# Optimization experiments

Measured on AMD Instinct MI355X. Metric: run time of the kernel, lower is better.

The kernel has to match this reference:

```python
import jax, jax.numpy as jnp
import numpy as np

D_MODEL = 1024
N_HEAD = 16
D_HEAD = D_MODEL // N_HEAD


def setup_inputs() -> dict:
    key = jax.random.key(0)
    ks = jax.random.split(key, 5)
    x = jax.random.normal(ks[0], (4, 2048, D_MODEL), dtype=jnp.float32)
    # qkv linear: weight [3*d_model, d_model], bias [3*d_model] (torch convention)
    w_qkv = jax.random.normal(ks[1], (3 * D_MODEL, D_MODEL), dtype=jnp.float32) / np.sqrt(D_MODEL)
    b_qkv = jnp.zeros((3 * D_MODEL,), dtype=jnp.float32)
    w_proj = jax.random.normal(ks[2], (D_MODEL, D_MODEL), dtype=jnp.float32) / np.sqrt(D_MODEL)
    b_proj = jnp.zeros((D_MODEL,), dtype=jnp.float32)
    return {"x": x, "w_qkv": w_qkv, "b_qkv": b_qkv, "w_proj": w_proj, "b_proj": b_proj}


def reference(x, w_qkv, b_qkv, w_proj, b_proj):
    B, T, C = x.shape
    qkv = x @ w_qkv.T + b_qkv  # [B,T,3C]
    q, k, v = jnp.split(qkv, 3, axis=-1)
    # [B, H, T, Dh]
    q = q.reshape(B, T, N_HEAD, D_HEAD).transpose(0, 2, 1, 3)
    k = k.reshape(B, T, N_HEAD, D_HEAD).transpose(0, 2, 1, 3)
    v = v.reshape(B, T, N_HEAD, D_HEAD).transpose(0, 2, 1, 3)
    att = jnp.einsum('bhqd,bhkd->bhqk', q, k) / jnp.sqrt(jnp.float32(D_HEAD))
    causal = jnp.tril(jnp.ones((T, T), dtype=bool))  # [T,T]
    att = jnp.where(causal, att, -jnp.inf)
    att = jax.nn.softmax(att, axis=-1)
    y = jnp.einsum('bhqk,bhkd->bhqd', att, v)  # [B,H,T,Dh]
    y = y.transpose(0, 2, 1, 3).reshape(B, T, C)
    return y @ w_proj.T + b_proj
```

## Files before the change

### kernel.cpp

```cpp
#include <hip/hip_runtime.h>
#include <hip/hip_bf16.h>

#define DEV static __device__ __forceinline__

typedef __attribute__((ext_vector_type(8))) short short8;
typedef __attribute__((ext_vector_type(4))) short short4v;
typedef __attribute__((ext_vector_type(4))) float float4v;
typedef __attribute__((ext_vector_type(4))) int int4v;

DEV unsigned short f2bf(float f) {
  unsigned int u = __builtin_bit_cast(unsigned int, f);
  u = (u + 0x7fffu + ((u >> 16) & 1u)) >> 16;
  return (unsigned short)u;
}

DEV __attribute__((address_space(3))) void* to_lds(void* p) {
  return (__attribute__((address_space(3))) void*)p;
}
DEV const __attribute__((address_space(1))) void* to_glb(const void* p) {
  return (const __attribute__((address_space(1))) void*)p;
}

DEV float4v zero4() { float4v z = {0.f, 0.f, 0.f, 0.f}; return z; }

DEV float ex2(float x) {
  float r;
  asm("v_exp_f32 %0, %1" : "=v"(r) : "v"(x));
  return r;
}
DEV unsigned int cvtpk(float lo, float hi) {
  unsigned int r;
  asm("v_cvt_pk_bf16_f32 %0, %1, %2" : "=v"(r) : "v"(lo), "v"(hi));
  return r;
}

__global__ __launch_bounds__(256)
void f32_to_bf16_kn(const float* __restrict__ src, unsigned short* __restrict__ dst, int n) {
  int i = (blockIdx.x * blockDim.x + threadIdx.x) * 4;
  int stride = gridDim.x * blockDim.x * 4;
  for (; i < n; i += stride) {
    float4v v = *reinterpret_cast<const float4v*>(src + i);
    short4v o;
    o[0] = (short)f2bf(v[0]);
    o[1] = (short)f2bf(v[1]);
    o[2] = (short)f2bf(v[2]);
    o[3] = (short)f2bf(v[3]);
    *reinterpret_cast<short4v*>(dst + i) = o;
  }
}

template<int BN, int WM, int WN, int EPI>
DEV void gemm256_body(const unsigned short* __restrict__ A, const unsigned short* __restrict__ B,
                      const float* __restrict__ bias, void* __restrict__ Cout,
                      unsigned short* __restrict__ vtout, int M, int N, int K,
                      unsigned short* sAraw, unsigned short* sBraw) {
  constexpr int MF = 256 / (WM * 16);
  constexpr int NF = BN / (WN * 16);
  constexpr int BPASS = BN / 64;
  const int t = threadIdx.x;
  const int lane = t & 63;
  const int wid = t >> 6;
  const int l15 = lane & 15, l4 = lane >> 4;
  const int wm = wid / WN, wn = wid % WN;
  const int wrow = wm * MF * 16, wcol = wn * NF * 16;
  const int gx = gridDim.x;
  const int nwg = gx * gridDim.y;
  const int lid = blockIdx.y * gx + blockIdx.x;
  const int swz = (lid & 7) * (nwg >> 3) + (lid >> 3);
  const int m0 = (swz / gx) * 256, n0 = (swz % gx) * BN;
  const int lkey = (l15 & 7) << 4;

  float4v acc[MF][NF];
#pragma unroll
  for (int i = 0; i < MF; i++)
#pragma unroll
    for (int j = 0; j < NF; j++) acc[i][j] = zero4();

  auto stage = [&](int bi, int k0) {
#pragma unroll
    for (int i = 0; i < 4; i++) {
      int unit = t + i * 512;
      int row = unit >> 3, sl = unit & 7;
      const unsigned short* g = &A[(size_t)(m0 + row) * K + k0 + (sl ^ (row & 7)) * 8];
      __builtin_amdgcn_global_load_lds(to_glb(g), to_lds(&sAraw[bi * 256 * 64 + unit * 8]), 16, 0, 0);
    }
#pragma unroll
    for (int i = 0; i < BPASS; i++) {
      int unit = t + i * 512;
      int row = unit >> 3, sl = unit & 7;
      const unsigned short* g = &B[(size_t)(n0 + row) * K + k0 + (sl ^ (row & 7)) * 8];
      __builtin_amdgcn_global_load_lds(to_glb(g), to_lds(&sBraw[bi * BN * 64 + unit * 8]), 16, 0, 0);
    }
  };

  stage(0, 0);
  const int nk = K >> 6;
  for (int s = 0; s < nk; ++s) {
    const int cur = s & 1;
    if (s + 1 < nk) {
      stage(cur ^ 1, (s + 1) << 6);
      if constexpr (BPASS == 3)
        asm volatile("s_waitcnt vmcnt(7)");
      else
        asm volatile("s_waitcnt vmcnt(6)");
    } else {
      asm volatile("s_waitcnt vmcnt(0)");
    }
    __builtin_amdgcn_sched_barrier(0);
    __builtin_amdgcn_s_barrier();
    __builtin_amdgcn_sched_barrier(0);

    const char* Ab = (const char*)&sAraw[cur * 256 * 64];
    const char* Bb = (const char*)&sBraw[cur * BN * 64];
    short8 bfr[NF][2];
#pragma unroll
    for (int nf = 0; nf < NF; nf++)
#pragma unroll
      for (int kc = 0; kc < 2; kc++) {
        int off = ((wcol + nf * 16 + l15) * 128 + kc * 64 + l4 * 16) ^ lkey;
        bfr[nf][kc] = *reinterpret_cast<const short8*>(Bb + off);
      }
#pragma unroll
    for (int g = 0; g < MF; g += 4) {
      short8 afr[4][2];
#pragma unroll
      for (int i = 0; i < 4; i++)
#pragma unroll
        for (int kc = 0; kc < 2; kc++) {
          int off = ((wrow + (g + i) * 16 + l15) * 128 + kc * 64 + l4 * 16) ^ lkey;
          afr[i][kc] = *reinterpret_cast<const short8*>(Ab + off);
        }
      __builtin_amdgcn_s_setprio(1);
#pragma unroll
      for (int kc = 0; kc < 2; kc++)
#pragma unroll
        for (int i = 0; i < 4; i++)
#pragma unroll
          for (int nf = 0; nf < NF; nf++)
            acc[g + i][nf] =
                __builtin_amdgcn_mfma_f32_16x16x32_bf16(afr[i][kc], bfr[nf][kc], acc[g + i][nf], 0, 0, 0);
      __builtin_amdgcn_s_setprio(0);
    }
    asm volatile("s_waitcnt lgkmcnt(0)" ::: "memory");
    __builtin_amdgcn_sched_barrier(0);
    __builtin_amdgcn_s_barrier();
    __builtin_amdgcn_sched_barrier(0);
  }

#pragma unroll
  for (int mf = 0; mf < MF; mf++) {
    const int row0 = m0 + wrow + mf * 16 + l4 * 4;
#pragma unroll
    for (int nf = 0; nf < NF; nf++) {
      const int col = n0 + wcol + nf * 16 + l15;
      float vv[4];
#pragma unroll
      for (int r = 0; r < 4; r++) vv[r] = acc[mf][nf][r] + bias[col];
      if (EPI == 1) {
#pragma unroll
        for (int r = 0; r < 4; r++)
          ((float*)Cout)[(size_t)(row0 + r) * N + col] = vv[r];
      } else {
        if (col < 2048) {
          const float sc = (col < 1024) ? 0.18033688f : 1.0f;
#pragma unroll
          for (int r = 0; r < 4; r++)
            ((unsigned short*)Cout)[(size_t)(row0 + r) * 2048 + col] = f2bf(vv[r] * sc);
        } else {
          const int hv = col - 2048;
          const int R = ((row0 >> 11) * 16 + (hv >> 6)) * 64 + (hv & 63);
          const int tc = row0 & 2047;
          unsigned long long w = (unsigned long long)cvtpk(vv[0], vv[1]) |
                                 ((unsigned long long)cvtpk(vv[2], vv[3]) << 32);
          *(unsigned long long*)&vtout[(size_t)R * 2048 + tc] = w;
        }
      }
    }
  }
}

__global__ __launch_bounds__(512, 2)
void gemm256_qkv_kn(const unsigned short* __restrict__ A, const unsigned short* __restrict__ B,
                    const float* __restrict__ bias, unsigned short* __restrict__ qkout,
                    unsigned short* __restrict__ vtout, int M, int N, int K) {
  __shared__ unsigned short sA[2][256 * 64];
  __shared__ unsigned short sB[2][192 * 64];
  gemm256_body<192, 2, 4, 2>(A, B, bias, qkout, vtout, M, N, K, &sA[0][0], &sB[0][0]);
}

__global__ __launch_bounds__(512, 2)
void gemm256_proj_kn(const unsigned short* __restrict__ A, const unsigned short* __restrict__ B,
                     const float* __restrict__ bias, float* __restrict__ Cout,
                     int M, int N, int K) {
  __shared__ unsigned short sA[2][256 * 64];
  __shared__ unsigned short sB[2][128 * 64];
  gemm256_body<128, 4, 2, 1>(A, B, bias, Cout, nullptr, M, N, K, &sA[0][0], &sB[0][0]);
}

__global__ __launch_bounds__(256, 3)
void attn_kn(const unsigned short* __restrict__ qk, const unsigned short* __restrict__ vt,
             unsigned short* __restrict__ y) {
  __shared__ unsigned short sK[2][4096];
  __shared__ unsigned short sV[2][4096];
  __shared__ unsigned short sP[4][2048];
  const int t = threadIdx.x;
  const int wave = t >> 6, lane = t & 63;
  const int l15 = lane & 15, l4 = lane >> 4;
  const int bh = blockIdx.x, b = bh >> 4, h = bh & 15;
  const int yb_ = blockIdx.y;
  const int qt = ((yb_ >> 2) & 1) ? ((yb_ < 8) ? yb_ + 4 : yb_ - 12) : 15 - yb_;
  const int q0w = qt * 128 + wave * 32;
  const size_t base = (size_t)b * 2048 * 2048;
  const unsigned short* Qp = qk + base + h * 64;
  const unsigned short* Kp = Qp + 1024;
  const unsigned short* Vt = vt + (size_t)bh * 64 * 2048;
  unsigned short* yb = y + (size_t)b * 2048 * 1024 + h * 64;

  short8 ones8;
#pragma unroll
  for (int j = 0; j < 8; j++) ones8[j] = (short)0x3F80;

  short8 qf[2][2];
#pragma unroll
  for (int m = 0; m < 2; m++)
#pragma unroll
    for (int kc = 0; kc < 2; kc++)
      qf[m][kc] = *reinterpret_cast<const short8*>(
          &Qp[(size_t)(q0w + m * 16 + l15) * 2048 + kc * 32 + l4 * 8]);

  float4v o_acc[2][4];
#pragma unroll
  for (int m = 0; m < 2; m++)
#pragma unroll
    for (int f = 0; f < 4; f++) o_acc[m][f] = zero4();
  float4v acc_l[2] = {zero4(), zero4()};

  auto stage_k = [&](int kv0, int bi) {
#pragma unroll
    for (int i = 0; i < 2; i++) {
      int unit = t + i * 256;
      int row = unit >> 3, sl = unit & 7;
      const unsigned short* g = Kp + (size_t)(kv0 + row) * 2048 + (sl ^ (row & 7)) * 8;
      __builtin_amdgcn_global_load_lds(to_glb(g), to_lds(&sK[bi][unit * 8]), 16, 0, 0);
    }
  };
  auto stage_v = [&](int kv0, int bi) {
#pragma unroll
    for (int i = 0; i < 2; i++) {
      int unit = t + i * 256;
      int d = unit >> 3, sl = unit & 7;
      const unsigned short* g = Vt + (size_t)d * 2048 + kv0 + (sl ^ (d & 7)) * 8;
      __builtin_amdgcn_global_load_lds(to_glb(g), to_lds(&sV[bi][unit * 8]), 16, 0, 0);
    }
  };

  const int nt = 2 * qt + 2;
  stage_k(0, 0);
  stage_v(0, 0);
  __syncthreads();

  for (int ti = 0; ti < nt; ti++) {
    const int cur = ti & 1;
    const int kv0 = ti * 64;
    const bool last = (ti + 1 == nt);
    if (!last) { stage_k(kv0 + 64, cur ^ 1); stage_v(kv0 + 64, cur ^ 1); }

    if (kv0 <= q0w + 31) {
      const char* Kb = (const char*)sK[cur];
      const char* Vb = (const char*)sV[cur];
      char* Pb = (char*)sP[wave];

      float4v st[2][4];
#pragma unroll
      for (int m = 0; m < 2; m++)
#pragma unroll
        for (int c = 0; c < 4; c++) st[m][c] = zero4();
#pragma unroll
      for (int kc = 0; kc < 2; kc++) {
        short8 ka[4];
#pragma unroll
        for (int c = 0; c < 4; c++) {
          int off = ((c * 16 + l15) * 128 + kc * 64 + l4 * 16) ^ ((l15 & 7) << 4);
          ka[c] = *reinterpret_cast<const short8*>(Kb + off);
        }
        __builtin_amdgcn_s_setprio(1);
#pragma unroll
        for (int c = 0; c < 4; c++) {
          st[0][c] = __builtin_amdgcn_mfma_f32_16x16x32_bf16(ka[c], qf[0][kc], st[0][c], 0, 0, 0);
          st[1][c] = __builtin_amdgcn_mfma_f32_16x16x32_bf16(ka[c], qf[1][kc], st[1][c], 0, 0, 0);
        }
        __builtin_amdgcn_s_setprio(0);
      }

#pragma unroll
      for (int m = 0; m < 2; m++) {
        if (kv0 + 63 > q0w + m * 16) {
          const int qrow = q0w + m * 16 + l15;
#pragma unroll
          for (int c = 0; c < 4; c++)
#pragma unroll
            for (int r = 0; r < 4; r++) {
              int kv = kv0 + c * 16 + l4 * 4 + r;
              if (kv > qrow) st[m][c][r] = -1e30f;
            }
        }
#pragma unroll
        for (int c = 0; c < 4; c++) {
          float p0 = ex2(st[m][c][0]), p1 = ex2(st[m][c][1]);
          float p2 = ex2(st[m][c][2]), p3 = ex2(st[m][c][3]);
          unsigned long long w = (unsigned long long)cvtpk(p0, p1) |
                                 ((unsigned long long)cvtpk(p2, p3) << 32);
          int off = ((m * 16 + l15) * 128 + (c * 16 + l4 * 4) * 2) ^ ((l15 & 7) << 4);
          *(unsigned long long*)(Pb + off) = w;
        }
      }
      asm volatile("s_waitcnt lgkmcnt(0)" ::: "memory");
      __builtin_amdgcn_sched_barrier(0);

#pragma unroll
      for (int kc = 0; kc < 2; kc++) {
        short8 pa[2];
#pragma unroll
        for (int m = 0; m < 2; m++) {
          int off = ((m * 16 + l15) * 128 + kc * 64 + l4 * 16) ^ ((l15 & 7) << 4);
          pa[m] = *reinterpret_cast<const short8*>(Pb + off);
        }
        short8 vbf[4];
#pragma unroll
        for (int f = 0; f < 4; f++) {
          int d = f * 16 + l15;
          int off = (d * 128 + kc * 64 + l4 * 16) ^ ((d & 7) << 4);
          vbf[f] = *reinterpret_cast<const short8*>(Vb + off);
        }
        __builtin_amdgcn_s_setprio(1);
#pragma unroll
        for (int f = 0; f < 4; f++) {
          o_acc[0][f] = __builtin_amdgcn_mfma_f32_16x16x32_bf16(pa[0], vbf[f], o_acc[0][f], 0, 0, 0);
          o_acc[1][f] = __builtin_amdgcn_mfma_f32_16x16x32_bf16(pa[1], vbf[f], o_acc[1][f], 0, 0, 0);
        }
        acc_l[0] = __builtin_amdgcn_mfma_f32_16x16x32_bf16(pa[0], ones8, acc_l[0], 0, 0, 0);
        acc_l[1] = __builtin_amdgcn_mfma_f32_16x16x32_bf16(pa[1], ones8, acc_l[1], 0, 0, 0);
        __builtin_amdgcn_s_setprio(0);
      }
    }
    __syncthreads();
  }

#pragma unroll
  for (int m = 0; m < 2; m++) {
    float lr[4];
#pragma unroll
    for (int r = 0; r < 4; r++) lr[r] = 1.0f / acc_l[m][r];
#pragma unroll
    for (int f = 0; f < 4; f++)
#pragma unroll
      for (int r = 0; r < 4; r++) {
        int q = q0w + m * 16 + l4 * 4 + r;
        yb[(size_t)q * 1024 + f * 16 + l15] = f2bf(o_acc[m][f][r] * lr[r]);
      }
  }
}

extern "C" void kernel_launch(void* const* d_in, const int* in_sizes, int n_in,
                              void* d_out, int out_size, void* d_ws, size_t ws_size,
                              hipStream_t stream) {
  const float* x = (const float*)d_in[0];
  const float* w_qkv = (const float*)d_in[1];
  const float* b_qkv = (const float*)d_in[2];
  const float* w_proj = (const float*)d_in[3];
  const float* b_proj = (const float*)d_in[4];
  float* out = (float*)d_out;
  char* ws = (char*)d_ws;

  const int M = 4 * 2048;
  unsigned short* x_bf = (unsigned short*)ws;
  unsigned short* wqkv_bf = (unsigned short*)(ws + (22ull << 20));
  unsigned short* wproj_bf = (unsigned short*)(ws + (28ull << 20));
  unsigned short* qk_buf = (unsigned short*)(ws + (30ull << 20));
  unsigned short* vt = (unsigned short*)(ws + (62ull << 20));
  unsigned short* y_bf = x_bf;

  f32_to_bf16_kn<<<2048, 256, 0, stream>>>(x, x_bf, M * 1024);
  f32_to_bf16_kn<<<1024, 256, 0, stream>>>(w_qkv, wqkv_bf, 3072 * 1024);
  f32_to_bf16_kn<<<512, 256, 0, stream>>>(w_proj, wproj_bf, 1024 * 1024);

  gemm256_qkv_kn<<<dim3(16, 32), 512, 0, stream>>>(
      x_bf, wqkv_bf, b_qkv, qk_buf, vt, M, 3072, 1024);

  attn_kn<<<dim3(64, 16), 256, 0, stream>>>(qk_buf, vt, y_bf);

  gemm256_proj_kn<<<dim3(8, 32), 512, 0, stream>>>(
      y_bf, wproj_bf, b_proj, out, M, 1024, 1024);
}
```

Baseline: 157.7 us.

## Rework GEMMs to K=32 tiles with wider QKV N-tile and new swizzle

Both GEMMs now stage K-slices of 32 instead of 64 with a new XOR swizzle. The QKV GEMM widens its N tile from 192 to 384, so it launches half as many blocks (256). The grid swizzle for L2 locality is removed and blocks map directly to tiles. Smaller K-steps halve shared-memory use per stage but double the number of barriers. The larger QKV tile adds register pressure and leaves fewer blocks to fill the CUs.

```diff
diff --git a/kernel.cpp b/kernel.cpp
--- a/kernel.cpp
+++ b/kernel.cpp
@@ -49,96 +49,84 @@
   }
 }
 
-template<int BN, int WM, int WN, int EPI>
-DEV void gemm256_body(const unsigned short* __restrict__ A, const unsigned short* __restrict__ B,
-                      const float* __restrict__ bias, void* __restrict__ Cout,
-                      unsigned short* __restrict__ vtout, int M, int N, int K,
-                      unsigned short* sAraw, unsigned short* sBraw) {
+template<int WM, int WN, int NFW, int EPI>
+DEV void gemm32_body(const unsigned short* __restrict__ A, const unsigned short* __restrict__ B,
+                     const float* __restrict__ bias, void* __restrict__ Cout,
+                     unsigned short* __restrict__ vtout, int M, int N, int K,
+                     unsigned short* sA, unsigned short* sB) {
+  constexpr int BN = WN * NFW * 16;
   constexpr int MF = 256 / (WM * 16);
-  constexpr int NF = BN / (WN * 16);
-  constexpr int BPASS = BN / 64;
-  const int t = threadIdx.x;
-  const int lane = t & 63;
-  const int wid = t >> 6;
+  constexpr int BPASS = BN / 128;
+  constexpr int L = 2 + BPASS;
+  const int t = threadIdx.x, lane = t & 63, wid = t >> 6;
   const int l15 = lane & 15, l4 = lane >> 4;
   const int wm = wid / WN, wn = wid % WN;
-  const int wrow = wm * MF * 16, wcol = wn * NF * 16;
-  const int gx = gridDim.x;
-  const int nwg = gx * gridDim.y;
-  const int lid = blockIdx.y * gx + blockIdx.x;
-  const int swz = (lid & 7) * (nwg >> 3) + (lid >> 3);
-  const int m0 = (swz / gx) * 256, n0 = (swz % gx) * BN;
-  const int lkey = (l15 & 7) << 4;
-
-  float4v acc[MF][NF];
+  const int wrow = wm * MF * 16, wcol = wn * NFW * 16;
+  const int m0 = blockIdx.y * 256, n0 = blockIdx.x * BN;
+
+  float4v acc[MF][NFW];
 #pragma unroll
   for (int i = 0; i < MF; i++)
 #pragma unroll
-    for (int j = 0; j < NF; j++) acc[i][j] = zero4();
-
-  auto stage = [&](int bi, int k0) {
-#pragma unroll
-    for (int i = 0; i < 4; i++) {
-      int unit = t + i * 512;
-      int row = unit >> 3, sl = unit & 7;
-      const unsigned short* g = &A[(size_t)(m0 + row) * K + k0 + (sl ^ (row & 7)) * 8];
-      __builtin_amdgcn_global_load_lds(to_glb(g), to_lds(&sAraw[bi * 256 * 64 + unit * 8]), 16, 0, 0);
-    }
-#pragma unroll
-    for (int i = 0; i < BPASS; i++) {
-      int unit = t + i * 512;
-      int row = unit >> 3, sl = unit & 7;
-      const unsigned short* g = &B[(size_t)(n0 + row) * K + k0 + (sl ^ (row & 7)) * 8];
-      __builtin_amdgcn_global_load_lds(to_glb(g), to_lds(&sBraw[bi * BN * 64 + unit * 8]), 16, 0, 0);
+    for (int j = 0; j < NFW; j++) acc[i][j] = zero4();
+
+  auto stage = [&](int buf, int k0) {
+#pragma unroll
+    for (int p = 0; p < 2; p++) {
+      int u = t + p * 512, row = u >> 2, sl = u & 3;
+      const unsigned short* g = &A[(size_t)(m0 + row) * K + k0 + (sl ^ ((row >> 1) & 3)) * 8];
+      __builtin_amdgcn_global_load_lds(to_glb(g), to_lds(&sA[buf * 256 * 32 + u * 8]), 16, 0, 0);
+    }
+#pragma unroll
+    for (int p = 0; p < BPASS; p++) {
+      int u = t + p * 512, row = u >> 2, sl = u & 3;
+      const unsigned short* g = &B[(size_t)(n0 + row) * K + k0 + (sl ^ ((row >> 1) & 3)) * 8];
+      __builtin_amdgcn_global_load_lds(to_glb(g), to_lds(&sB[buf * BN * 32 + u * 8]), 16, 0, 0);
     }
   };
 
   stage(0, 0);
-  const int nk = K >> 6;
+  const int nk = K >> 5;
   for (int s = 0; s < nk; ++s) {
     const int cur = s & 1;
     if (s + 1 < nk) {
-      stage(cur ^ 1, (s + 1) << 6);
-      if constexpr (BPASS == 3)
-        asm volatile("s_waitcnt vmcnt(7)");
+      stage(cur ^ 1, (s + 1) << 5);
+      if constexpr (L == 5)
+        asm volatile("s_waitcnt vmcnt(5)" ::: "memory");
       else
-        asm volatile("s_waitcnt vmcnt(6)");
+        asm volatile("s_waitcnt vmcnt(3)" ::: "memory");
     } else {
-      asm volatile("s_waitcnt vmcnt(0)");
+      asm volatile("s_waitcnt vmcnt(0)" ::: "memory");
     }
     __builtin_amdgcn_sched_barrier(0);
     __builtin_amdgcn_s_barrier();
     __builtin_amdgcn_sched_barrier(0);
 
-    const char* Ab = (const char*)&sAraw[cur * 256 * 64];
-    const char* Bb = (const char*)&sBraw[cur * BN * 64];
-    short8 bfr[NF][2];
-#pragma unroll
-    for (int nf = 0; nf < NF; nf++)
-#pragma unroll
-      for (int kc = 0; kc < 2; kc++) {
-        int off = ((wcol + nf * 16 + l15) * 128 + kc * 64 + l4 * 16) ^ lkey;
-        bfr[nf][kc] = *reinterpret_cast<const short8*>(Bb + off);
-      }
-#pragma unroll
-    for (int g = 0; g < MF; g += 4) {
-      short8 afr[4][2];
-#pragma unroll
-      for (int i = 0; i < 4; i++)
-#pragma unroll
-        for (int kc = 0; kc < 2; kc++) {
-          int off = ((wrow + (g + i) * 16 + l15) * 128 + kc * 64 + l4 * 16) ^ lkey;
-          afr[i][kc] = *reinterpret_cast<const short8*>(Ab + off);
-        }
+    const char* Ab = (const char*)&sA[cur * 256 * 32];
+    const char* Bb = (const char*)&sB[cur * BN * 32];
+    short8 bfr[NFW];
+#pragma unroll
+    for (int nf = 0; nf < NFW; nf++) {
+      int row = wcol + nf * 16 + l15;
+      int off = row * 64 + ((l4 ^ ((row >> 1) & 3)) << 4);
+      bfr[nf] = *reinterpret_cast<const short8*>(Bb + off);
+    }
+#pragma unroll
+    for (int g = 0; g < MF; g += 2) {
+      short8 af[2];
+#pragma unroll
+      for (int i = 0; i < 2; i++) {
+        int row = wrow + (g + i) * 16 + l15;
+        int off = row * 64 + ((l4 ^ ((row >> 1) & 3)) << 4);
+        af[i] = *reinterpret_cast<const short8*>(Ab + off);
+      }
       __builtin_amdgcn_s_setprio(1);
 #pragma unroll
-      for (int kc = 0; kc < 2; kc++)
-#pragma unroll
-        for (int i = 0; i < 4; i++)
-#pragma unroll
-          for (int nf = 0; nf < NF; nf++)
-            acc[g + i][nf] =
-                __builtin_amdgcn_mfma_f32_16x16x32_bf16(afr[i][kc], bfr[nf][kc], acc[g + i][nf], 0, 0, 0);
+      for (int i = 0; i < 2; i++)
+#pragma unroll
+        for (int nf = 0; nf < NFW; nf++)
+          acc[g + i][nf] =
+              __builtin_amdgcn_mfma_f32_16x16x32_bf16(af[i], bfr[nf], acc[g + i][nf], 0, 0, 0);
       __builtin_amdgcn_s_setprio(0);
     }
     asm volatile("s_waitcnt lgkmcnt(0)" ::: "memory");
@@ -151,7 +139,7 @@
   for (int mf = 0; mf < MF; mf++) {
     const int row0 = m0 + wrow + mf * 16 + l4 * 4;
 #pragma unroll
-    for (int nf = 0; nf < NF; nf++) {
+    for (int nf = 0; nf < NFW; nf++) {
       const int col = n0 + wcol + nf * 16 + l15;
       float vv[4];
 #pragma unroll
@@ -180,21 +168,21 @@
 }
 
 __global__ __launch_bounds__(512, 2)
-void gemm256_qkv_kn(const unsigned short* __restrict__ A, const unsigned short* __restrict__ B,
-                    const float* __restrict__ bias, unsigned short* __restrict__ qkout,
-                    unsigned short* __restrict__ vtout, int M, int N, int K) {
-  __shared__ unsigned short sA[2][256 * 64];
-  __shared__ unsigned short sB[2][192 * 64];
-  gemm256_body<192, 2, 4, 2>(A, B, bias, qkout, vtout, M, N, K, &sA[0][0], &sB[0][0]);
+void gemm32_qkv_kn(const unsigned short* __restrict__ A, const unsigned short* __restrict__ B,
+                   const float* __restrict__ bias, unsigned short* __restrict__ qkout,
+                   unsigned short* __restrict__ vtout, int M, int N, int K) {
+  __shared__ unsigned short sA[2 * 256 * 32];
+  __shared__ unsigned short sB[2 * 384 * 32];
+  gemm32_body<2, 4, 6, 2>(A, B, bias, qkout, vtout, M, N, K, sA, sB);
 }
 
 __global__ __launch_bounds__(512, 2)
-void gemm256_proj_kn(const unsigned short* __restrict__ A, const unsigned short* __restrict__ B,
-                     const float* __restrict__ bias, float* __restrict__ Cout,
-                     int M, int N, int K) {
-  __shared__ unsigned short sA[2][256 * 64];
-  __shared__ unsigned short sB[2][128 * 64];
-  gemm256_body<128, 4, 2, 1>(A, B, bias, Cout, nullptr, M, N, K, &sA[0][0], &sB[0][0]);
+void gemm32_proj_kn(const unsigned short* __restrict__ A, const unsigned short* __restrict__ B,
+                    const float* __restrict__ bias, float* __restrict__ Cout,
+                    int M, int N, int K) {
+  __shared__ unsigned short sA[2 * 256 * 32];
+  __shared__ unsigned short sB[2 * 128 * 32];
+  gemm32_body<4, 2, 4, 1>(A, B, bias, Cout, nullptr, M, N, K, sA, sB);
 }
 
 __global__ __launch_bounds__(256, 3)
@@ -384,11 +372,11 @@
   f32_to_bf16_kn<<<1024, 256, 0, stream>>>(w_qkv, wqkv_bf, 3072 * 1024);
   f32_to_bf16_kn<<<512, 256, 0, stream>>>(w_proj, wproj_bf, 1024 * 1024);
 
-  gemm256_qkv_kn<<<dim3(16, 32), 512, 0, stream>>>(
+  gemm32_qkv_kn<<<dim3(8, 32), 512, 0, stream>>>(
       x_bf, wqkv_bf, b_qkv, qk_buf, vt, M, 3072, 1024);
 
   attn_kn<<<dim3(64, 16), 256, 0, stream>>>(qk_buf, vt, y_bf);
 
-  gemm256_proj_kn<<<dim3(8, 32), 512, 0, stream>>>(
+  gemm32_proj_kn<<<dim3(8, 32), 512, 0, stream>>>(
       y_bf, wproj_bf, b_proj, out, M, 1024, 1024);
 }
```

New measurement: 167.5 us. 6.2% more time.
